# Optimization experiments

Measured on AMD Instinct MI355X. Metric: run time of the kernel, lower is better.

## Reference

```python
import jax, jax.numpy as jnp
import numpy as np

N = 131072      # total nodes
B = 16          # graphs in batch (num_segments)
C = 128         # in_channels
K = 16          # n_super_nodes
TAU = 1.0
PRUNING_THRESHOLD = 0.01
SPARSITY_WEIGHT = 0.01
TEMPORAL_W = 0.1 * 5
COLLAPSE_W = 2.0
EPS = 1e-9


def setup_inputs() -> dict:
    key = jax.random.key(0)
    ks = jax.random.split(key, 8)
    x = jax.random.normal(ks[0], (N, C), dtype=jnp.float32)
    batch = jnp.sort(jax.random.randint(ks[1], (N,), 0, B)).astype(jnp.int64)
    pos = jax.random.normal(ks[2], (N, 2), dtype=jnp.float32)
    # Gumbel noise for gumbel_softmax (sampled once, passed as input for determinism)
    gumbel = jax.random.gumbel(ks[3], (N, K), dtype=jnp.float32)
    # assign_mlp params: Linear(C,C) -> ReLU -> Linear(C,K)
    W1 = jax.random.normal(ks[4], (C, C), dtype=jnp.float32) / np.sqrt(C)
    b1 = jnp.zeros((C,), dtype=jnp.float32)
    W2 = jax.random.normal(ks[5], (K, C), dtype=jnp.float32) / np.sqrt(C)
    b2 = jnp.zeros((K,), dtype=jnp.float32)
    scaling = jnp.asarray(10.0, dtype=jnp.float32)
    active_mask = jnp.ones((K,), dtype=jnp.float32)  # buffer, starts all-active
    return {"x": x, "batch": batch, "pos": pos, "gumbel": gumbel,
            "W1": W1, "b1": b1, "W2": W2, "b2": b2,
            "scaling": scaling, "active_mask": active_mask}


def reference(x, batch, pos, gumbel, W1, b1, W2, b2, scaling, active_mask):
    # --- assignment logits: MLP * scaling (eval mode, prev_assignments=None) ---
    h = jax.nn.relu(x @ W1.T + b1)            # [N, C]
    logits = (h @ W2.T + b2) * scaling        # [N, K]
    # eval-path masking: masked_fill(mask == 0, -1e9)
    masked_logits = jnp.where(active_mask[None, :] == 0.0, -1e9, logits)
    # gumbel_softmax (soft, hard=False)
    s = jax.nn.softmax((masked_logits + gumbel) / TAU, axis=-1)   # [N, K]

    avg_s = jnp.mean(s, axis=0)               # [K]

    # --- losses ---
    entropy = -jnp.mean(jnp.sum(s * jnp.log(s + EPS), axis=1))
    uniform_p = 1.0 / K
    diversity = jnp.sum(uniform_p * jnp.log(uniform_p / (avg_s + EPS)))
    pruning = jnp.mean(jnp.abs(avg_s * (1.0 - active_mask)))
    sparsity = (jnp.sum(active_mask) / K) * SPARSITY_WEIGHT
    temporal = jnp.asarray(0.0, jnp.float32)  # prev_assignments is None
    # collapse-prevention / balance bodies are truncated upstream; faithful proxies
    collapse = jnp.sum((avg_s - uniform_p) ** 2) * COLLAPSE_W
    balance = jnp.std(avg_s)
    spatial = jnp.asarray(0.0, jnp.float32)

    # --- pooled features: out[b,k,c] = sum_{n in graph b} s[n,k] * x[n,c] ---
    weighted = x[:, None, :] * s[:, :, None]                  # [N, K, C]
    out = jax.ops.segment_sum(weighted, batch, num_segments=B)  # [B, K, C]

    # --- super-node positions ---
    w_pos = pos[:, None, :] * s[:, :, None]                    # [N, K, 2]
    sum_s_pos = jax.ops.segment_sum(w_pos, batch, num_segments=B)  # [B, K, 2]
    sum_s = jax.ops.segment_sum(s, batch, num_segments=B)[..., None] + EPS  # [B, K, 1]
    mu = sum_s_pos / sum_s                                     # [B, K, 2]

    # --- separation loss: pairwise repulsion between super-node centers ---
    dist_sq = jnp.sum((mu[:, :, None, :] - mu[:, None, :, :]) ** 2, axis=-1)  # [B,K,K]
    eye = jnp.eye(K, dtype=mu.dtype)[None]
    repulsion = 1.0 / (dist_sq + 1.0)
    separation = jnp.sum(repulsion * (1.0 - eye)) / (K * (K - 1))

    losses = jnp.stack([entropy, diversity, spatial, pruning, sparsity,
                        temporal * TEMPORAL_W, collapse, balance, separation])
    return out, s, mu, losses
```

## Files before the change

kernel.cpp:

```cpp
#include <hip/hip_runtime.h>
#include <hip/hip_bf16.h>
#include <math.h>

#define NN 131072
#define BSEG 16
#define CCH 128
#define KK 16
#define EPSF 1e-9f
#define XST 136

#define OFF_S   32768
#define OFF_MU  2129920
#define OFF_L   2130432

#define FLAG_IDX 800
#define REDC_BASE 1024
#define REDC_STRIDE 1024
#define NRED 64
#define ST_BASE (REDC_BASE + NRED * REDC_STRIDE)
#define NST 4
#define ST_SZ (BSEG * KK * CCH)

typedef __bf16 bf16x8 __attribute__((ext_vector_type(8)));
typedef float  f32x4  __attribute__((ext_vector_type(4)));
typedef float  f32x16 __attribute__((ext_vector_type(16)));

__device__ __forceinline__ int load_batch(const void* bptr, int n, int is64) {
    if (is64) return (int)((const long long*)bptr)[n];
    return ((const int*)bptr)[n];
}

__device__ __forceinline__ float wave_sum(float v) {
#pragma unroll
    for (int o = 32; o > 0; o >>= 1) v += __shfl_xor(v, o, 64);
    return v;
}

__device__ __forceinline__ bf16x8 pack8(float4 a, float4 b) {
    bf16x8 v;
    v[0] = (__bf16)a.x; v[1] = (__bf16)a.y; v[2] = (__bf16)a.z; v[3] = (__bf16)a.w;
    v[4] = (__bf16)b.x; v[5] = (__bf16)b.y; v[6] = (__bf16)b.z; v[7] = (__bf16)b.w;
    return v;
}

__global__ void k_zero(float* __restrict__ ws, const int* __restrict__ b32) {
    int i = blockIdx.x * 256 + threadIdx.x;
    ws[REDC_BASE + i] = 0.0f;
    if (i == 0) ws[FLAG_IDX] = (b32[NN - 1] == 0) ? 1.0f : 0.0f;
}

__global__ __launch_bounds__(512, 4) void k_fused(
    const float* __restrict__ x, const void* __restrict__ batch,
    const float* __restrict__ pos, const float* __restrict__ gumbel,
    const float* __restrict__ W1, const float* __restrict__ b1,
    const float* __restrict__ W2, const float* __restrict__ b2,
    const float* __restrict__ scaling, const float* __restrict__ active_mask,
    float* __restrict__ s_out, float* __restrict__ ws)
{
    __shared__ __align__(16) __bf16 x_lds[128 * XST];
    __shared__ __align__(16) __bf16 h_lds[128 * XST];
    __shared__ __align__(16) __bf16 sT[16 * XST];
    __shared__ int bsegs[128];

    const int tid  = threadIdx.x;
    const int lane = tid & 63;
    const int wv   = tid >> 6;
    const int n0   = blockIdx.x * 128;
    const int is64 = (int)ws[FLAG_IDX];

    if (tid < 128) bsegs[tid] = load_batch(batch, n0 + tid, is64);

    float4 ga0, ga1, ga2, ga3;
    if (tid < 128) {
        const float4* gp = (const float4*)(gumbel + (size_t)(n0 + tid) * KK);
        ga0 = gp[0]; ga1 = gp[1]; ga2 = gp[2]; ga3 = gp[3];
    }

    {
        const float4* xg = (const float4*)(x + (size_t)n0 * CCH);
#pragma unroll
        for (int i = 0; i < 4; i++) {
            int p = i * 512 + tid;
            float4 a = xg[2 * p], b = xg[2 * p + 1];
            *(bf16x8*)&x_lds[(p >> 4) * XST + (p & 15) * 8] = pack8(a, b);
        }
    }
    __syncthreads();

    {
        const int jw  = wv & 3;
        const int mth = wv >> 2;
        bf16x8 bfr[8];
        const float* wrow = W1 + (size_t)(jw * 32 + (lane & 31)) * CCH + (lane >> 5) * 8;
#pragma unroll
        for (int ks = 0; ks < 8; ks++) {
            float4 u = *(const float4*)(wrow + ks * 16);
            float4 v = *(const float4*)(wrow + ks * 16 + 4);
            bfr[ks] = pack8(u, v);
        }
        f32x16 acc[2];
#pragma unroll
        for (int t = 0; t < 2; t++)
#pragma unroll
            for (int r = 0; r < 16; r++) acc[t][r] = 0.0f;

#pragma unroll
        for (int ks = 0; ks < 8; ks++) {
#pragma unroll
            for (int t = 0; t < 2; t++) {
                int mt = mth * 2 + t;
                bf16x8 a = *(bf16x8*)&x_lds[(size_t)(mt * 32 + (lane & 31)) * XST + ks * 16 + (lane >> 5) * 8];
                acc[t] = __builtin_amdgcn_mfma_f32_32x32x16_bf16(a, bfr[ks], acc[t], 0, 0, 0);
            }
        }
        const float b1j = b1[jw * 32 + (lane & 31)];
#pragma unroll
        for (int t = 0; t < 2; t++)
#pragma unroll
            for (int r = 0; r < 16; r++) {
                int node = (mth * 2 + t) * 32 + (r & 3) + 8 * (r >> 2) + 4 * (lane >> 5);
                h_lds[(size_t)node * XST + jw * 32 + (lane & 31)] = (__bf16)fmaxf(acc[t][r] + b1j, 0.0f);
            }
    }
    __syncthreads();

    {
        f32x4 acc2;
#pragma unroll
        for (int r = 0; r < 4; r++) acc2[r] = 0.0f;

#pragma unroll
        for (int ks = 0; ks < 4; ks++) {
            const float* w2row = W2 + (size_t)(lane & 15) * CCH + ks * 32 + (lane >> 4) * 8;
            float4 u = *(const float4*)w2row;
            float4 v = *(const float4*)(w2row + 4);
            bf16x8 bw = pack8(u, v);
            bf16x8 a = *(bf16x8*)&h_lds[(size_t)(wv * 16 + (lane & 15)) * XST + ks * 32 + (lane >> 4) * 8];
            acc2 = __builtin_amdgcn_mfma_f32_16x16x32_bf16(a, bw, acc2, 0, 0, 0);
        }
#pragma unroll
        for (int r = 0; r < 4; r++) {
            int node = wv * 16 + (lane >> 4) * 4 + r;
            float* lp = (float*)((char*)h_lds + (size_t)node * (XST * 2) + 192);
            lp[lane & 15] = acc2[r];
        }
    }
    __syncthreads();

    if (tid < 128) {
        const int n = n0 + tid;
        const char* rb = (const char*)h_lds + (size_t)tid * (XST * 2);
        float lg[16], gu[16];
#pragma unroll
        for (int i = 0; i < 4; i++) {
            float4 t = *(const float4*)(rb + 192 + 16 * i);
            lg[4 * i] = t.x; lg[4 * i + 1] = t.y; lg[4 * i + 2] = t.z; lg[4 * i + 3] = t.w;
        }
        gu[0] = ga0.x; gu[1] = ga0.y; gu[2]  = ga0.z; gu[3]  = ga0.w;
        gu[4] = ga1.x; gu[5] = ga1.y; gu[6]  = ga1.z; gu[7]  = ga1.w;
        gu[8] = ga2.x; gu[9] = ga2.y; gu[10] = ga2.z; gu[11] = ga2.w;
        gu[12] = ga3.x; gu[13] = ga3.y; gu[14] = ga3.z; gu[15] = ga3.w;

        const float sc = scaling[0];
        float m = -1e30f;
#pragma unroll
        for (int k = 0; k < KK; k++) {
            float v = (lg[k] + b2[k]) * sc;
            if (active_mask[k] == 0.0f) v = -1e9f;
            v += gu[k];
            lg[k] = v;
            m = fmaxf(m, v);
        }
        float ssum = 0.0f;
#pragma unroll
        for (int k = 0; k < KK; k++) { lg[k] = expf(lg[k] - m); ssum += lg[k]; }
        const float inv = 1.0f / ssum;
        float sarr[16];
#pragma unroll
        for (int k = 0; k < KK; k++) sarr[k] = lg[k] * inv;

        float4* srow = (float4*)(s_out + (size_t)n * KK);
#pragma unroll
        for (int i = 0; i < 4; i++) {
            float4 t;
            t.x = sarr[4 * i]; t.y = sarr[4 * i + 1]; t.z = sarr[4 * i + 2]; t.w = sarr[4 * i + 3];
            srow[i] = t;
        }
#pragma unroll
        for (int k = 0; k < KK; k++) sT[k * XST + tid] = (__bf16)sarr[k];

        float ent = 0.0f;
#pragma unroll
        for (int k = 0; k < KK; k++) ent += sarr[k] * logf(sarr[k] + EPSF);

        const float2 p = ((const float2*)pos)[n];
        const int bi = bsegs[tid];
        const int b0 = __shfl(bi, 0, 64);
        const int b1s = __shfl(bi, 63, 64);
        const float prim = (bi == b0) ? 1.0f : 0.0f;
        float* rc = ws + REDC_BASE + (size_t)(blockIdx.x & (NRED - 1)) * REDC_STRIDE;

#pragma unroll
        for (int k = 0; k < KK; k++) {
            float v = wave_sum(sarr[k] * prim);
            if (lane == 0) atomicAdd(&rc[b0 * 16 + k], v);
        }
#pragma unroll
        for (int k = 0; k < KK; k++) {
            float vx = wave_sum(sarr[k] * p.x * prim);
            float vy = wave_sum(sarr[k] * p.y * prim);
            if (lane == 0) {
                atomicAdd(&rc[256 + b0 * 32 + 2 * k],     vx);
                atomicAdd(&rc[256 + b0 * 32 + 2 * k + 1], vy);
            }
        }
        {
            float e = wave_sum(ent * prim);
            if (lane == 0) atomicAdd(&rc[768], e);
        }

        if (b0 != b1s) {
            const float sec = 1.0f - prim;
#pragma unroll
            for (int k = 0; k < KK; k++) {
                float v = wave_sum(sarr[k] * sec);
                if (lane == 0) atomicAdd(&rc[b1s * 16 + k], v);
            }
#pragma unroll
            for (int k = 0; k < KK; k++) {
                float vx = wave_sum(sarr[k] * p.x * sec);
                float vy = wave_sum(sarr[k] * p.y * sec);
                if (lane == 0) {
                    atomicAdd(&rc[256 + b1s * 32 + 2 * k],     vx);
                    atomicAdd(&rc[256 + b1s * 32 + 2 * k + 1], vy);
                }
            }
            float e = wave_sum(ent * sec);
            if (lane == 0) atomicAdd(&rc[768], e);
        }
    }
    __syncthreads();

    {
        float* stg = ws + ST_BASE + (size_t)(blockIdx.x & (NST - 1)) * ST_SZ;
        const int bfirst = bsegs[0], blast = bsegs[127];
        for (int seg = bfirst; seg <= blast; seg++) {
            const bool masked = (bfirst != blast);
            f32x4 pacc;
#pragma unroll
            for (int r = 0; r < 4; r++) pacc[r] = 0.0f;

#pragma unroll
            for (int ks = 0; ks < 4; ks++) {
                bf16x8 a = *(bf16x8*)&sT[(size_t)(lane & 15) * XST + ks * 32 + (lane >> 4) * 8];
                if (masked) {
#pragma unroll
                    for (int i = 0; i < 8; i++) {
                        int nd = ks * 32 + (lane >> 4) * 8 + i;
                        if (bsegs[nd] != seg) a[i] = (__bf16)0.0f;
                    }
                }
                bf16x8 bx;
#pragma unroll
                for (int i = 0; i < 8; i++)
                    bx[i] = x_lds[(size_t)(ks * 32 + (lane >> 4) * 8 + i) * XST + wv * 16 + (lane & 15)];
                pacc = __builtin_amdgcn_mfma_f32_16x16x32_bf16(a, bx, pacc, 0, 0, 0);
            }
            const int c = wv * 16 + (lane & 15);
#pragma unroll
            for (int r = 0; r < 4; r++) {
                int k = (lane >> 4) * 4 + r;
                atomicAdd(&stg[((size_t)seg * KK + k) * CCH + c], pacc[r]);
            }
        }
    }
}

__global__ __launch_bounds__(256) void k_reduce(
    const float* __restrict__ ws, float* __restrict__ out,
    const float* __restrict__ active_mask,
    float* __restrict__ mu_out, float* __restrict__ losses)
{
    const int tid = threadIdx.x;
    if (blockIdx.x < 32) {
        int i = blockIdx.x * 256 + tid;
        const float4* s0 = (const float4*)(ws + ST_BASE);
        const float4* s1 = (const float4*)(ws + ST_BASE + ST_SZ);
        const float4* s2 = (const float4*)(ws + ST_BASE + 2 * ST_SZ);
        const float4* s3 = (const float4*)(ws + ST_BASE + 3 * ST_SZ);
        float4 a = s0[i], b = s1[i], c = s2[i], d = s3[i];
        float4 r;
        r.x = (a.x + b.x) + (c.x + d.x);
        r.y = (a.y + b.y) + (c.y + d.y);
        r.z = (a.z + b.z) + (c.z + d.z);
        r.w = (a.w + b.w) + (c.w + d.w);
        ((float4*)out)[i] = r;
        return;
    }

    __shared__ float lsum[256];
    __shared__ float lpos[512];
    __shared__ float lent;
    __shared__ float smu[512];
    __shared__ float savg[16];
    __shared__ float red[256];

    for (int a = tid; a < 769; a += 256) {
        float acc = 0.0f;
#pragma unroll 8
        for (int c = 0; c < NRED; c++) acc += ws[REDC_BASE + c * REDC_STRIDE + a];
        if (a < 256) lsum[a] = acc;
        else if (a < 768) lpos[a - 256] = acc;
        else lent = acc;
    }
    __syncthreads();

    if (tid < 16) {
        float a = 0.0f;
#pragma unroll
        for (int b = 0; b < 16; b++) a += lsum[b * 16 + tid];
        savg[tid] = a / (float)NN;
    }
    for (int i = tid; i < 512; i += 256) {
        int sk = i >> 1;
        float v = lpos[i] / (lsum[sk] + EPSF);
        smu[i] = v;
        mu_out[i] = v;
    }
    __syncthreads();

    float rep = 0.0f;
    for (int t = tid; t < 4096; t += 256) {
        int b = t >> 8, i = (t >> 4) & 15, j = t & 15;
        if (i != j) {
            float dx = smu[b * 32 + i * 2]     - smu[b * 32 + j * 2];
            float dy = smu[b * 32 + i * 2 + 1] - smu[b * 32 + j * 2 + 1];
            rep += 1.0f / (dx * dx + dy * dy + 1.0f);
        }
    }
    red[tid] = rep;
    __syncthreads();
    for (int st = 128; st > 0; st >>= 1) {
        if (tid < st) red[tid] += red[tid + st];
        __syncthreads();
    }

    if (tid == 0) {
        const float p = 1.0f / 16.0f;
        float separation = red[0] / (float)(16 * 15);
        float entropy = -lent / (float)NN;
        float diversity = 0.f, pruning = 0.f, amsum = 0.f, collapse = 0.f, mean = 0.f;
        for (int k = 0; k < 16; k++) {
            float a = savg[k];
            diversity += p * logf(p / (a + EPSF));
            pruning += fabsf(a * (1.0f - active_mask[k]));
            amsum += active_mask[k];
            collapse += (a - p) * (a - p);
            mean += a;
        }
        pruning /= 16.0f;
        mean /= 16.0f;
        float var = 0.f;
        for (int k = 0; k < 16; k++) { float d = savg[k] - mean; var += d * d; }
        float balance = sqrtf(var / 16.0f);
        float sparsity = (amsum / 16.0f) * 0.01f;
        collapse *= 2.0f;
        losses[0] = entropy;   losses[1] = diversity; losses[2] = 0.0f;
        losses[3] = pruning;   losses[4] = sparsity;  losses[5] = 0.0f;
        losses[6] = collapse;  losses[7] = balance;   losses[8] = separation;
    }
}

extern "C" void kernel_launch(void* const* d_in, const int* in_sizes, int n_in,
                              void* d_out, int out_size, void* d_ws, size_t ws_size,
                              hipStream_t stream) {
    const float* x       = (const float*)d_in[0];
    const void*  batch   = d_in[1];
    const float* pos     = (const float*)d_in[2];
    const float* gumbel  = (const float*)d_in[3];
    const float* W1      = (const float*)d_in[4];
    const float* b1      = (const float*)d_in[5];
    const float* W2      = (const float*)d_in[6];
    const float* b2      = (const float*)d_in[7];
    const float* scaling = (const float*)d_in[8];
    const float* am      = (const float*)d_in[9];

    float* out      = (float*)d_out;
    float* s_sec    = out + OFF_S;
    float* mu_sec   = out + OFF_MU;
    float* loss_sec = out + OFF_L;
    float* wsf      = (float*)d_ws;

    k_zero<<<768, 256, 0, stream>>>(wsf, (const int*)batch);
    k_fused<<<NN / 128, 512, 0, stream>>>(x, batch, pos, gumbel, W1, b1, W2, b2,
                                          scaling, am, s_sec, wsf);
    k_reduce<<<33, 256, 0, stream>>>(wsf, out, am, mu_sec, loss_sec);
}
```

Before: 189.3 us.

## Replace pooled-feature atomics with per-block bf16 partials reduced by segment range

Each fused block now writes its pooled K×C partial sums, split into a first-segment part and a remainder part, as bf16 into a per-block slot instead of atomically adding fp32 into four staging copies. The reduce kernel binary-searches segment boundaries in the batch array and sums only the tiles belonging to each segment. The softmax entropy is computed analytically from the logits with fast exp/log, and the is64 flag is computed inline so k_zero clears less memory. This removes many global float atomics and shrinks zeroing, at the cost of bf16 rounding of partials and an assumption that a 128-node tile spans at most two segments.

After: 196.6 us. +3.8%, slower.

```diff
diff --git a/kernel.cpp b/kernel.cpp
--- a/kernel.cpp
+++ b/kernel.cpp
@@ -8,20 +8,19 @@
 #define KK 16
 #define EPSF 1e-9f
 #define XST 136
+#define BN 128
+#define NBLK (NN / BN)
 
 #define OFF_S   32768
 #define OFF_MU  2129920
 #define OFF_L   2130432
 
-#define FLAG_IDX 800
-#define REDC_BASE 1024
+#define NRED 64
 #define REDC_STRIDE 1024
-#define NRED 64
-#define ST_BASE (REDC_BASE + NRED * REDC_STRIDE)
-#define NST 4
-#define ST_SZ (BSEG * KK * CCH)
+#define POOL_OFF_BYTES 262144
 
 typedef __bf16 bf16x8 __attribute__((ext_vector_type(8)));
+typedef __bf16 bf16x4 __attribute__((ext_vector_type(4)));
 typedef float  f32x4  __attribute__((ext_vector_type(4)));
 typedef float  f32x16 __attribute__((ext_vector_type(16)));
 
@@ -43,10 +42,9 @@
     return v;
 }
 
-__global__ void k_zero(float* __restrict__ ws, const int* __restrict__ b32) {
+__global__ void k_zero(float* __restrict__ ws) {
     int i = blockIdx.x * 256 + threadIdx.x;
-    ws[REDC_BASE + i] = 0.0f;
-    if (i == 0) ws[FLAG_IDX] = (b32[NN - 1] == 0) ? 1.0f : 0.0f;
+    ((float4*)ws)[i] = make_float4(0.f, 0.f, 0.f, 0.f);
 }
 
 __global__ __launch_bounds__(512, 4) void k_fused(
@@ -55,23 +53,25 @@
     const float* __restrict__ W1, const float* __restrict__ b1,
     const float* __restrict__ W2, const float* __restrict__ b2,
     const float* __restrict__ scaling, const float* __restrict__ active_mask,
-    float* __restrict__ s_out, float* __restrict__ ws)
+    float* __restrict__ s_out, float* __restrict__ redc, __bf16* __restrict__ pool)
 {
-    __shared__ __align__(16) __bf16 x_lds[128 * XST];
-    __shared__ __align__(16) __bf16 h_lds[128 * XST];
+    __shared__ __align__(16) __bf16 x_lds[BN * XST];
+    __shared__ __align__(16) __bf16 h_lds[BN * XST];
     __shared__ __align__(16) __bf16 sT[16 * XST];
-    __shared__ int bsegs[128];
+    __shared__ int bsegs[BN];
+    __shared__ int nb_sh;
 
     const int tid  = threadIdx.x;
     const int lane = tid & 63;
     const int wv   = tid >> 6;
-    const int n0   = blockIdx.x * 128;
-    const int is64 = (int)ws[FLAG_IDX];
-
-    if (tid < 128) bsegs[tid] = load_batch(batch, n0 + tid, is64);
+    const int n0   = blockIdx.x * BN;
+    const int is64 = (((const int*)batch)[NN - 1] == 0) ? 1 : 0;
+
+    if (tid == 0) nb_sh = BN;
+    if (tid < BN) bsegs[tid] = load_batch(batch, n0 + tid, is64);
 
     float4 ga0, ga1, ga2, ga3;
-    if (tid < 128) {
+    if (tid < BN) {
         const float4* gp = (const float4*)(gumbel + (size_t)(n0 + tid) * KK);
         ga0 = gp[0]; ga1 = gp[1]; ga2 = gp[2]; ga3 = gp[3];
     }
@@ -86,6 +86,8 @@
         }
     }
     __syncthreads();
+
+    if (tid > 0 && tid < BN && bsegs[tid] != bsegs[tid - 1]) nb_sh = tid;
 
     {
         const int jw  = wv & 3;
@@ -147,7 +149,7 @@
     }
     __syncthreads();
 
-    if (tid < 128) {
+    if (tid < BN) {
         const int n = n0 + tid;
         const char* rb = (const char*)h_lds + (size_t)tid * (XST * 2);
         float lg[16], gu[16];
@@ -172,12 +174,14 @@
             m = fmaxf(m, v);
         }
         float ssum = 0.0f;
-#pragma unroll
-        for (int k = 0; k < KK; k++) { lg[k] = expf(lg[k] - m); ssum += lg[k]; }
+        float sarr[16];
+#pragma unroll
+        for (int k = 0; k < KK; k++) { sarr[k] = __expf(lg[k] - m); ssum += sarr[k]; }
         const float inv = 1.0f / ssum;
-        float sarr[16];
-#pragma unroll
-        for (int k = 0; k < KK; k++) sarr[k] = lg[k] * inv;
+        float sdotl = 0.0f;
+#pragma unroll
+        for (int k = 0; k < KK; k++) { sarr[k] *= inv; sdotl = fmaf(sarr[k], lg[k], sdotl); }
+        const float ent = sdotl - m - __logf(ssum);
 
         float4* srow = (float4*)(s_out + (size_t)n * KK);
 #pragma unroll
@@ -188,17 +192,13 @@
         }
 #pragma unroll
         for (int k = 0; k < KK; k++) sT[k * XST + tid] = (__bf16)sarr[k];
-
-        float ent = 0.0f;
-#pragma unroll
-        for (int k = 0; k < KK; k++) ent += sarr[k] * logf(sarr[k] + EPSF);
 
         const float2 p = ((const float2*)pos)[n];
         const int bi = bsegs[tid];
         const int b0 = __shfl(bi, 0, 64);
         const int b1s = __shfl(bi, 63, 64);
         const float prim = (bi == b0) ? 1.0f : 0.0f;
-        float* rc = ws + REDC_BASE + (size_t)(blockIdx.x & (NRED - 1)) * REDC_STRIDE;
+        float* rc = redc + (size_t)(blockIdx.x & (NRED - 1)) * REDC_STRIDE;
 
 #pragma unroll
         for (int k = 0; k < KK; k++) {
@@ -242,59 +242,91 @@
     __syncthreads();
 
     {
-        float* stg = ws + ST_BASE + (size_t)(blockIdx.x & (NST - 1)) * ST_SZ;
-        const int bfirst = bsegs[0], blast = bsegs[127];
-        for (int seg = bfirst; seg <= blast; seg++) {
-            const bool masked = (bfirst != blast);
-            f32x4 pacc;
-#pragma unroll
-            for (int r = 0; r < 4; r++) pacc[r] = 0.0f;
-
+        const int nb = nb_sh;
+        f32x4 pall, p0;
+#pragma unroll
+        for (int r = 0; r < 4; r++) { pall[r] = 0.0f; p0[r] = 0.0f; }
+
+#pragma unroll
+        for (int ks = 0; ks < 4; ks++) {
+            bf16x8 a = *(bf16x8*)&sT[(size_t)(lane & 15) * XST + ks * 32 + (lane >> 4) * 8];
+            bf16x8 bx;
+#pragma unroll
+            for (int i = 0; i < 8; i++)
+                bx[i] = x_lds[(size_t)(ks * 32 + (lane >> 4) * 8 + i) * XST + wv * 16 + (lane & 15)];
+            pall = __builtin_amdgcn_mfma_f32_16x16x32_bf16(a, bx, pall, 0, 0, 0);
+        }
+        if (nb != BN) {
 #pragma unroll
             for (int ks = 0; ks < 4; ks++) {
                 bf16x8 a = *(bf16x8*)&sT[(size_t)(lane & 15) * XST + ks * 32 + (lane >> 4) * 8];
-                if (masked) {
-#pragma unroll
-                    for (int i = 0; i < 8; i++) {
-                        int nd = ks * 32 + (lane >> 4) * 8 + i;
-                        if (bsegs[nd] != seg) a[i] = (__bf16)0.0f;
-                    }
+#pragma unroll
+                for (int i = 0; i < 8; i++) {
+                    int nd = ks * 32 + (lane >> 4) * 8 + i;
+                    if (nd >= nb) a[i] = (__bf16)0.0f;
                 }
                 bf16x8 bx;
 #pragma unroll
                 for (int i = 0; i < 8; i++)
                     bx[i] = x_lds[(size_t)(ks * 32 + (lane >> 4) * 8 + i) * XST + wv * 16 + (lane & 15)];
-                pacc = __builtin_amdgcn_mfma_f32_16x16x32_bf16(a, bx, pacc, 0, 0, 0);
-            }
-            const int c = wv * 16 + (lane & 15);
-#pragma unroll
-            for (int r = 0; r < 4; r++) {
-                int k = (lane >> 4) * 4 + r;
-                atomicAdd(&stg[((size_t)seg * KK + k) * CCH + c], pacc[r]);
-            }
-        }
-    }
+                p0 = __builtin_amdgcn_mfma_f32_16x16x32_bf16(a, bx, p0, 0, 0, 0);
+            }
+        } else {
+            p0 = pall;
+        }
+        __bf16* slot = pool + (size_t)blockIdx.x * 4096;
+        const int c = wv * 16 + (lane & 15);
+#pragma unroll
+        for (int r = 0; r < 4; r++) {
+            int k = (lane >> 4) * 4 + r;
+            slot[k * CCH + c]        = (__bf16)p0[r];
+            slot[2048 + k * CCH + c] = (__bf16)(pall[r] - p0[r]);
+        }
+    }
+}
+
+__device__ __forceinline__ int lower_bound_seg(const void* batch, int is64, int s) {
+    if (s <= 0) return 0;
+    if (s > BSEG - 1) return NN;
+    int lo = 0, hi = NN;
+    while (lo < hi) {
+        int mid = (lo + hi) >> 1;
+        int v = load_batch(batch, mid, is64);
+        if (v < s) lo = mid + 1; else hi = mid;
+    }
+    return lo;
 }
 
 __global__ __launch_bounds__(256) void k_reduce(
-    const float* __restrict__ ws, float* __restrict__ out,
+    const float* __restrict__ ws, const __bf16* __restrict__ pool,
+    const void* __restrict__ batch, float* __restrict__ out,
     const float* __restrict__ active_mask,
     float* __restrict__ mu_out, float* __restrict__ losses)
 {
     const int tid = threadIdx.x;
+    const int is64 = (((const int*)batch)[NN - 1] == 0) ? 1 : 0;
+
     if (blockIdx.x < 32) {
-        int i = blockIdx.x * 256 + tid;
-        const float4* s0 = (const float4*)(ws + ST_BASE);
-        const float4* s1 = (const float4*)(ws + ST_BASE + ST_SZ);
-        const float4* s2 = (const float4*)(ws + ST_BASE + 2 * ST_SZ);
-        const float4* s3 = (const float4*)(ws + ST_BASE + 3 * ST_SZ);
-        float4 a = s0[i], b = s1[i], c = s2[i], d = s3[i];
-        float4 r;
-        r.x = (a.x + b.x) + (c.x + d.x);
-        r.y = (a.y + b.y) + (c.y + d.y);
-        r.z = (a.z + b.z) + (c.z + d.z);
-        r.w = (a.w + b.w) + (c.w + d.w);
-        ((float4*)out)[i] = r;
+        __shared__ int lb[3];
+        const int b    = blockIdx.x >> 1;
+        const int half = blockIdx.x & 1;
+        if (tid < 3) lb[tid] = lower_bound_seg(batch, is64, b - 1 + tid);
+        __syncthreads();
+        const int tlo0 = (lb[1] + BN - 1) >> 7, thi0 = (lb[2] + BN - 1) >> 7;
+        const int tlo1 = (lb[0] + BN - 1) >> 7, thi1 = (lb[1] + BN - 1) >> 7;
+
+        const int e0 = half * 1024 + tid * 4;
+        float a0 = 0.f, a1 = 0.f, a2 = 0.f, a3 = 0.f;
+        for (int t = tlo0; t < thi0; t++) {
+            bf16x4 v = *(const bf16x4*)&pool[(size_t)t * 4096 + e0];
+            a0 += (float)v[0]; a1 += (float)v[1]; a2 += (float)v[2]; a3 += (float)v[3];
+        }
+        for (int t = tlo1; t < thi1; t++) {
+            bf16x4 v = *(const bf16x4*)&pool[(size_t)t * 4096 + 2048 + e0];
+            a0 += (float)v[0]; a1 += (float)v[1]; a2 += (float)v[2]; a3 += (float)v[3];
+        }
+        float* ob = out + (size_t)b * 2048 + e0;
+        ob[0] = a0; ob[1] = a1; ob[2] = a2; ob[3] = a3;
         return;
     }
 
@@ -308,7 +340,7 @@
     for (int a = tid; a < 769; a += 256) {
         float acc = 0.0f;
 #pragma unroll 8
-        for (int c = 0; c < NRED; c++) acc += ws[REDC_BASE + c * REDC_STRIDE + a];
+        for (int c = 0; c < NRED; c++) acc += ws[c * REDC_STRIDE + a];
         if (a < 256) lsum[a] = acc;
         else if (a < 768) lpos[a - 256] = acc;
         else lent = acc;
@@ -390,9 +422,10 @@
     float* mu_sec   = out + OFF_MU;
     float* loss_sec = out + OFF_L;
     float* wsf      = (float*)d_ws;
-
-    k_zero<<<768, 256, 0, stream>>>(wsf, (const int*)batch);
-    k_fused<<<NN / 128, 512, 0, stream>>>(x, batch, pos, gumbel, W1, b1, W2, b2,
-                                          scaling, am, s_sec, wsf);
-    k_reduce<<<33, 256, 0, stream>>>(wsf, out, am, mu_sec, loss_sec);
-}
+    __bf16* pool    = (__bf16*)((char*)d_ws + POOL_OFF_BYTES);
+
+    k_zero<<<64, 256, 0, stream>>>(wsf);
+    k_fused<<<NBLK, 512, 0, stream>>>(x, batch, pos, gumbel, W1, b1, W2, b2,
+                                      scaling, am, s_sec, wsf, pool);
+    k_reduce<<<33, 256, 0, stream>>>(wsf, pool, batch, out, am, mu_sec, loss_sec);
+}
```
